# Kernel tuning notes

Hardware: AMD Instinct MI355X
Metric: run time of the kernel (lower is better)

The kernel has to match this reference:

```python
import jax, jax.numpy as jnp
import numpy as np


def build_weights(target):
    """Vectorized version of the per-(batch,frame) distance-weight loop.

    target: [B, T, W, W]. For each frame, find the mean (row, col) coordinate
    of the maximal pixels, then weight = W / (dist_to_center + 1).
    """
    W = target.shape[-1]
    m = jnp.max(target, axis=(-2, -1), keepdims=True)
    mask = (target == m).astype(target.dtype)          # [B,T,W,W]
    cnt = jnp.sum(mask, axis=(-2, -1))                 # [B,T]
    idx = jnp.arange(W, dtype=target.dtype)            # [W]
    # mean row index x and mean col index y of argmax pixels
    x = jnp.sum(jnp.sum(mask, axis=-1) * idx, axis=-1) / cnt  # [B,T]
    y = jnp.sum(jnp.sum(mask, axis=-2) * idx, axis=-1) / cnt  # [B,T]
    a = idx[None, None, :, None] - x[:, :, None, None]  # row offsets [B,T,W,1]
    b = idx[None, None, None, :] - y[:, :, None, None]  # col offsets [B,T,1,W]
    dist = jnp.sqrt(a * a + b * b)                      # [B,T,W,W]
    return W / (dist + 1.0)  # reciprocal of (sqrt(dist)+1)/W


def setup_inputs() -> dict:
    key = jax.random.key(0)
    k1, k2 = jax.random.split(key)
    B, T, W = 16, 16, 256
    inp = jax.random.uniform(k1, (B, 1, T, W, W), dtype=jnp.float32)
    tgt = jax.random.uniform(k2, (B, T, W, W), dtype=jnp.float32)
    return {"input": inp, "target": tgt}


def reference(input, target):
    p = jnp.squeeze(input, axis=1)                 # [B,T,W,W]
    w = build_weights(target)
    # torch binary_cross_entropy clamps log terms at -100
    logp = jnp.clip(jnp.log(p), -100.0)
    log1mp = jnp.clip(jnp.log1p(-p), -100.0)
    loss = -jnp.mean(w * (target * logp + (1.0 - target) * log1mp))
    return loss
```

## Files before the change

kernel.cpp:

```cpp
#include <hip/hip_runtime.h>

#define WDIM 256
#define FRAME (WDIM * WDIM)
#define NFRAMES 256
#define NTOT ((long long)NFRAMES * FRAME)
#define NBLK 2048
#define SUBV4 2048


__global__ __launch_bounds__(256)
void floss_stats(const float* __restrict__ target, float4* __restrict__ blk) {
    const int bid = blockIdx.x;
    const int fid = bid >> 3, sub = bid & 7;
    const int tid = threadIdx.x;
    const int lane = tid & 63, wave = tid >> 6;

    const float4* __restrict__ t4 =
        (const float4*)(target + (size_t)fid * FRAME) + sub * SUBV4;

    float4 tv[8];
    #pragma unroll
    for (int k = 0; k < 8; ++k) tv[k] = t4[k * 256 + tid];

    float lmax = -1.0f;
    #pragma unroll
    for (int k = 0; k < 8; ++k)
        lmax = fmaxf(lmax, fmaxf(fmaxf(tv[k].x, tv[k].y), fmaxf(tv[k].z, tv[k].w)));

    float wm = lmax;
    #pragma unroll
    for (int off = 32; off > 0; off >>= 1) wm = fmaxf(wm, __shfl_down(wm, off));
    __shared__ float s_wm[4];
    __shared__ float s_st[4][3];
    if (lane == 0) s_wm[wave] = wm;
    __syncthreads();
    const float bmax = fmaxf(fmaxf(s_wm[0], s_wm[1]), fmaxf(s_wm[2], s_wm[3]));

    float cnt = 0.0f, sr = 0.0f, sc = 0.0f;
    const float rowb = (float)(sub * 32 + (tid >> 6));
    const float colb = (float)((tid & 63) * 4);
    #pragma unroll
    for (int k = 0; k < 8; ++k) {
        const float row = rowb + (float)(4 * k);
        const float vv[4] = {tv[k].x, tv[k].y, tv[k].z, tv[k].w};
        #pragma unroll
        for (int j = 0; j < 4; ++j)
            if (vv[j] == bmax) { cnt += 1.0f; sr += row; sc += colb + (float)j; }
    }
    #pragma unroll
    for (int off = 32; off > 0; off >>= 1) {
        cnt += __shfl_down(cnt, off);
        sr  += __shfl_down(sr,  off);
        sc  += __shfl_down(sc,  off);
    }
    if (lane == 0) { s_st[wave][0] = cnt; s_st[wave][1] = sr; s_st[wave][2] = sc; }
    __syncthreads();
    if (tid == 0) {
        float c = 0.0f, r = 0.0f, cc = 0.0f;
        #pragma unroll
        for (int w = 0; w < 4; ++w) { c += s_st[w][0]; r += s_st[w][1]; cc += s_st[w][2]; }
        blk[bid] = make_float4(bmax, c, r, cc);
    }
}

__global__ __launch_bounds__(256)
void floss_bce(const float* __restrict__ input, const float* __restrict__ target,
               const float4* __restrict__ blk, double* __restrict__ bsum) {
    const int bid = blockIdx.x;
    const int fid = bid >> 3, sub = bid & 7;
    const int tid = threadIdx.x;
    const int lane = tid & 63, wave = tid >> 6;

    const float4* __restrict__ t4 =
        (const float4*)(target + (size_t)fid * FRAME) + sub * SUBV4;
    const float4* __restrict__ p4 =
        (const float4*)(input + (size_t)fid * FRAME) + sub * SUBV4;

    float fm = -1.0f;
    float4 st[8];
    #pragma unroll
    for (int i = 0; i < 8; ++i) {
        st[i] = blk[(fid << 3) + i];
        fm = fmaxf(fm, st[i].x);
    }
    float cnt = 0.0f, sr = 0.0f, sc = 0.0f;
    #pragma unroll
    for (int i = 0; i < 8; ++i)
        if (st[i].x == fm) { cnt += st[i].y; sr += st[i].z; sc += st[i].w; }
    const float rc = __builtin_amdgcn_rcpf(cnt);
    const float x = sr * rc;
    const float y = sc * rc;

    const float rowb = (float)(sub * 32 + (tid >> 6));
    float dc2[4];
    #pragma unroll
    for (int j = 0; j < 4; ++j) {
        const float d = (float)((tid & 63) * 4 + j) - y;
        dc2[j] = d * d;
    }

    float acc0 = 0.0f, acc1 = 0.0f;
    #pragma unroll
    for (int k = 0; k < 8; ++k) {
        const float4 tv = t4[k * 256 + tid];
        const float4 pv = p4[k * 256 + tid];
        const float dr = rowb + (float)(4 * k) - x;
        const float dr2 = dr * dr;
        const float tt[4] = {tv.x, tv.y, tv.z, tv.w};
        const float pp[4] = {pv.x, pv.y, pv.z, pv.w};
        #pragma unroll
        for (int j = 0; j < 4; ++j) {
            const float dist = __builtin_amdgcn_sqrtf(dr2 + dc2[j]);
            const float w = 256.0f * __builtin_amdgcn_rcpf(dist + 1.0f);
            const float p = pp[j];
            const float lp  = fmaxf(__logf(p), -100.0f);
            const float l1p = fmaxf(__logf(1.0f - p), -100.0f);
            if (j & 1) acc1 += w * fmaf(tt[j], lp - l1p, l1p);
            else       acc0 += w * fmaf(tt[j], lp - l1p, l1p);
        }
    }

    float local = acc0 + acc1;
    #pragma unroll
    for (int off = 32; off > 0; off >>= 1) local += __shfl_down(local, off);
    __shared__ float s_acc[4];
    if (lane == 0) s_acc[wave] = local;
    __syncthreads();
    if (tid == 0)
        bsum[bid] = (double)(s_acc[0] + s_acc[1] + s_acc[2] + s_acc[3]);
}

__global__ __launch_bounds__(1024)
void floss_final(const double* __restrict__ bsum, float* __restrict__ out) {
    const int tid = threadIdx.x;
    const int lane = tid & 63, wave = tid >> 6;
    double v = bsum[tid] + bsum[tid + 1024];
    #pragma unroll
    for (int off = 32; off > 0; off >>= 1) v += __shfl_down(v, off);
    __shared__ double sd[16];
    if (lane == 0) sd[wave] = v;
    __syncthreads();
    if (tid == 0) {
        double s = 0.0;
        #pragma unroll
        for (int w = 0; w < 16; ++w) s += sd[w];
        out[0] = (float)(-s / (double)NTOT);
    }
}

extern "C" void kernel_launch(void* const* d_in, const int* in_sizes, int n_in,
                              void* d_out, int out_size, void* d_ws, size_t ws_size,
                              hipStream_t stream) {
    const float* input  = (const float*)d_in[0];
    const float* target = (const float*)d_in[1];
    float* out = (float*)d_out;
    float4* blk  = (float4*)d_ws;
    double* bsum = (double*)((char*)d_ws + NBLK * sizeof(float4));

    floss_stats<<<NBLK, 256, 0, stream>>>(target, blk);
    floss_bce<<<NBLK, 256, 0, stream>>>(input, target, blk, bsum);
    floss_final<<<1, 1024, 0, stream>>>(bsum, out);
}
```

Baseline: 145.5 us.

## Fuse stats, BCE and final reduction into one kernel with per-frame spin sync

Merges the three kernels into a single launch. The target tile is kept in registers as packed bf16 after the max pass, so the BCE pass does not reload target from memory. The eight blocks of each frame exchange argmax statistics through global atomics and a spin-wait, and the last block to finish does the final reduction. Input loads are double-buffered one step ahead. This removes one full read of target and two kernel launches, but adds a memset, a co-residency dependence for the spin-wait, and bf16 rounding of target in the loss.

```diff
diff --git a/kernel.cpp b/kernel.cpp
--- a/kernel.cpp
+++ b/kernel.cpp
@@ -1,4 +1,6 @@
 #include <hip/hip_runtime.h>
+#include <hip/hip_bf16.h>
+#include <string.h>
 
 #define WDIM 256
 #define FRAME (WDIM * WDIM)
@@ -8,64 +10,16 @@
 #define SUBV4 2048
 
 
-__global__ __launch_bounds__(256)
-void floss_stats(const float* __restrict__ target, float4* __restrict__ blk) {
-    const int bid = blockIdx.x;
-    const int fid = bid >> 3, sub = bid & 7;
-    const int tid = threadIdx.x;
-    const int lane = tid & 63, wave = tid >> 6;
-
-    const float4* __restrict__ t4 =
-        (const float4*)(target + (size_t)fid * FRAME) + sub * SUBV4;
-
-    float4 tv[8];
-    #pragma unroll
-    for (int k = 0; k < 8; ++k) tv[k] = t4[k * 256 + tid];
-
-    float lmax = -1.0f;
-    #pragma unroll
-    for (int k = 0; k < 8; ++k)
-        lmax = fmaxf(lmax, fmaxf(fmaxf(tv[k].x, tv[k].y), fmaxf(tv[k].z, tv[k].w)));
-
-    float wm = lmax;
-    #pragma unroll
-    for (int off = 32; off > 0; off >>= 1) wm = fmaxf(wm, __shfl_down(wm, off));
-    __shared__ float s_wm[4];
-    __shared__ float s_st[4][3];
-    if (lane == 0) s_wm[wave] = wm;
-    __syncthreads();
-    const float bmax = fmaxf(fmaxf(s_wm[0], s_wm[1]), fmaxf(s_wm[2], s_wm[3]));
-
-    float cnt = 0.0f, sr = 0.0f, sc = 0.0f;
-    const float rowb = (float)(sub * 32 + (tid >> 6));
-    const float colb = (float)((tid & 63) * 4);
-    #pragma unroll
-    for (int k = 0; k < 8; ++k) {
-        const float row = rowb + (float)(4 * k);
-        const float vv[4] = {tv[k].x, tv[k].y, tv[k].z, tv[k].w};
-        #pragma unroll
-        for (int j = 0; j < 4; ++j)
-            if (vv[j] == bmax) { cnt += 1.0f; sr += row; sc += colb + (float)j; }
-    }
-    #pragma unroll
-    for (int off = 32; off > 0; off >>= 1) {
-        cnt += __shfl_down(cnt, off);
-        sr  += __shfl_down(sr,  off);
-        sc  += __shfl_down(sc,  off);
-    }
-    if (lane == 0) { s_st[wave][0] = cnt; s_st[wave][1] = sr; s_st[wave][2] = sc; }
-    __syncthreads();
-    if (tid == 0) {
-        float c = 0.0f, r = 0.0f, cc = 0.0f;
-        #pragma unroll
-        for (int w = 0; w < 4; ++w) { c += s_st[w][0]; r += s_st[w][1]; cc += s_st[w][2]; }
-        blk[bid] = make_float4(bmax, c, r, cc);
-    }
+__device__ inline unsigned int pack_bf16x2(float a, float b) {
+    __hip_bfloat162 h = __float22bfloat162_rn(make_float2(a, b));
+    unsigned int u; memcpy(&u, &h, 4); return u;
 }
 
-__global__ __launch_bounds__(256)
-void floss_bce(const float* __restrict__ input, const float* __restrict__ target,
-               const float4* __restrict__ blk, double* __restrict__ bsum) {
+__global__ __launch_bounds__(256, 8)
+void floss_all(const float* __restrict__ input, const float* __restrict__ target,
+               int* arrive, int* done,
+               float4* __restrict__ blk, double* __restrict__ bsum,
+               float* __restrict__ out) {
     const int bid = blockIdx.x;
     const int fid = bid >> 3, sub = bid & 7;
     const int tid = threadIdx.x;
@@ -76,22 +30,76 @@
     const float4* __restrict__ p4 =
         (const float4*)(input + (size_t)fid * FRAME) + sub * SUBV4;
 
-    float fm = -1.0f;
-    float4 st[8];
+    __shared__ float s_wm[4];
+    __shared__ float s_cnt, s_sr, s_sc;
+    __shared__ float s_xy[2];
+    __shared__ float s_acc[4];
+    __shared__ double s_d[4];
+    __shared__ int s_last;
+
+    if (tid == 0) { s_cnt = 0.f; s_sr = 0.f; s_sc = 0.f; }
+
+    unsigned int st16[16];
+    float lmax = -1.f;
     #pragma unroll
-    for (int i = 0; i < 8; ++i) {
-        st[i] = blk[(fid << 3) + i];
-        fm = fmaxf(fm, st[i].x);
+    for (int k = 0; k < 8; ++k) {
+        const float4 v = t4[k * 256 + tid];
+        lmax = fmaxf(lmax, fmaxf(fmaxf(v.x, v.y), fmaxf(v.z, v.w)));
+        st16[2 * k]     = pack_bf16x2(v.x, v.y);
+        st16[2 * k + 1] = pack_bf16x2(v.z, v.w);
     }
-    float cnt = 0.0f, sr = 0.0f, sc = 0.0f;
+    float wm = lmax;
     #pragma unroll
-    for (int i = 0; i < 8; ++i)
-        if (st[i].x == fm) { cnt += st[i].y; sr += st[i].z; sc += st[i].w; }
-    const float rc = __builtin_amdgcn_rcpf(cnt);
-    const float x = sr * rc;
-    const float y = sc * rc;
+    for (int off = 32; off > 0; off >>= 1) wm = fmaxf(wm, __shfl_down(wm, off));
+    if (lane == 0) s_wm[wave] = wm;
+    __syncthreads();
+    const float bmax = fmaxf(fmaxf(s_wm[0], s_wm[1]), fmaxf(s_wm[2], s_wm[3]));
 
-    const float rowb = (float)(sub * 32 + (tid >> 6));
+    float4 pA = p4[tid], pB = p4[256 + tid];
+
+    if (lmax == bmax) {
+        float cnt = 0.f, sr = 0.f, sc = 0.f;
+        const float rowb = (float)(sub * 32 + wave);
+        const float colb = (float)((tid & 63) * 4);
+        for (int k = 0; k < 8; ++k) {
+            const float4 v = t4[k * 256 + tid];
+            const float row = rowb + (float)(4 * k);
+            const float vv[4] = {v.x, v.y, v.z, v.w};
+            #pragma unroll
+            for (int j = 0; j < 4; ++j)
+                if (vv[j] == bmax) { cnt += 1.f; sr += row; sc += colb + (float)j; }
+        }
+        atomicAdd(&s_cnt, cnt); atomicAdd(&s_sr, sr); atomicAdd(&s_sc, sc);
+    }
+    __syncthreads();
+
+    if (tid == 0) {
+        blk[bid] = make_float4(bmax, s_cnt, s_sr, s_sc);
+        __threadfence();
+        __hip_atomic_fetch_add(&arrive[fid], 1, __ATOMIC_RELEASE,
+                               __HIP_MEMORY_SCOPE_AGENT);
+        int spins = 0;
+        while (__hip_atomic_load(&arrive[fid], __ATOMIC_ACQUIRE,
+                                 __HIP_MEMORY_SCOPE_AGENT) < 8) {
+            __builtin_amdgcn_s_sleep(2);
+            if (++spins > (1 << 22)) break;
+        }
+        float4 r[8];
+        float fm = -1.f;
+        #pragma unroll
+        for (int i = 0; i < 8; ++i) { r[i] = blk[(fid << 3) + i]; fm = fmaxf(fm, r[i].x); }
+        float cnt = 0.f, sr = 0.f, sc = 0.f;
+        #pragma unroll
+        for (int i = 0; i < 8; ++i)
+            if (r[i].x == fm) { cnt += r[i].y; sr += r[i].z; sc += r[i].w; }
+        const float rc = __builtin_amdgcn_rcpf(cnt);
+        s_xy[0] = sr * rc;
+        s_xy[1] = sc * rc;
+    }
+    __syncthreads();
+
+    const float x = s_xy[0], y = s_xy[1];
+    const float rowb = (float)(sub * 32 + wave);
     float dc2[4];
     #pragma unroll
     for (int j = 0; j < 4; ++j) {
@@ -99,15 +107,22 @@
         dc2[j] = d * d;
     }
 
-    float acc0 = 0.0f, acc1 = 0.0f;
+    float acc0 = 0.f, acc1 = 0.f;
     #pragma unroll
     for (int k = 0; k < 8; ++k) {
-        const float4 tv = t4[k * 256 + tid];
-        const float4 pv = p4[k * 256 + tid];
+        const float4 pv = (k & 1) ? pB : pA;
+        if (k < 6) {
+            if (k & 1) pB = p4[(k + 2) * 256 + tid];
+            else       pA = p4[(k + 2) * 256 + tid];
+        }
+        const unsigned int w0 = st16[2 * k], w1 = st16[2 * k + 1];
+        const float tt[4] = {
+            __uint_as_float(w0 << 16), __uint_as_float(w0 & 0xffff0000u),
+            __uint_as_float(w1 << 16), __uint_as_float(w1 & 0xffff0000u)
+        };
+        const float pp[4] = {pv.x, pv.y, pv.z, pv.w};
         const float dr = rowb + (float)(4 * k) - x;
         const float dr2 = dr * dr;
-        const float tt[4] = {tv.x, tv.y, tv.z, tv.w};
-        const float pp[4] = {pv.x, pv.y, pv.z, pv.w};
         #pragma unroll
         for (int j = 0; j < 4; ++j) {
             const float dist = __builtin_amdgcn_sqrtf(dr2 + dc2[j]);
@@ -123,28 +138,28 @@
     float local = acc0 + acc1;
     #pragma unroll
     for (int off = 32; off > 0; off >>= 1) local += __shfl_down(local, off);
-    __shared__ float s_acc[4];
     if (lane == 0) s_acc[wave] = local;
     __syncthreads();
-    if (tid == 0)
+
+    if (tid == 0) {
         bsum[bid] = (double)(s_acc[0] + s_acc[1] + s_acc[2] + s_acc[3]);
-}
-
-__global__ __launch_bounds__(1024)
-void floss_final(const double* __restrict__ bsum, float* __restrict__ out) {
-    const int tid = threadIdx.x;
-    const int lane = tid & 63, wave = tid >> 6;
-    double v = bsum[tid] + bsum[tid + 1024];
-    #pragma unroll
-    for (int off = 32; off > 0; off >>= 1) v += __shfl_down(v, off);
-    __shared__ double sd[16];
-    if (lane == 0) sd[wave] = v;
+        __threadfence();
+        const int t = __hip_atomic_fetch_add(done, 1, __ATOMIC_ACQ_REL,
+                                             __HIP_MEMORY_SCOPE_AGENT);
+        s_last = (t == NBLK - 1) ? 1 : 0;
+    }
     __syncthreads();
-    if (tid == 0) {
-        double s = 0.0;
+    if (s_last) {
+        __threadfence();
+        double v = 0.0;
         #pragma unroll
-        for (int w = 0; w < 16; ++w) s += sd[w];
-        out[0] = (float)(-s / (double)NTOT);
+        for (int i = 0; i < 8; ++i) v += bsum[tid + 256 * i];
+        #pragma unroll
+        for (int off = 32; off > 0; off >>= 1) v += __shfl_down(v, off);
+        if (lane == 0) s_d[wave] = v;
+        __syncthreads();
+        if (tid == 0)
+            out[0] = (float)(-(s_d[0] + s_d[1] + s_d[2] + s_d[3]) / (double)NTOT);
     }
 }
 
@@ -154,10 +169,12 @@
     const float* input  = (const float*)d_in[0];
     const float* target = (const float*)d_in[1];
     float* out = (float*)d_out;
-    float4* blk  = (float4*)d_ws;
-    double* bsum = (double*)((char*)d_ws + NBLK * sizeof(float4));
 
-    floss_stats<<<NBLK, 256, 0, stream>>>(target, blk);
-    floss_bce<<<NBLK, 256, 0, stream>>>(input, target, blk, bsum);
-    floss_final<<<1, 1024, 0, stream>>>(bsum, out);
+    int* arrive  = (int*)d_ws;
+    int* done    = arrive + 256;
+    float4* blk  = (float4*)((char*)d_ws + 4096);
+    double* bsum = (double*)((char*)d_ws + 4096 + NBLK * sizeof(float4));
+
+    hipMemsetAsync(d_ws, 0, 4096, stream);
+    floss_all<<<NBLK, 256, 0, stream>>>(input, target, arrive, done, blk, bsum, out);
 }
```

Measured after the change: 515.3 us. 254% more time.
